# Kernel optimization log

Hardware: AMD Instinct MI355X
Metric: run time of the kernel (lower is better)

The kernel has to match this reference:

```python
import jax, jax.numpy as jnp
import numpy as np
from jax import lax
import math

B, T, CIN, H, W = 8, 64, 2, 64, 64
HID, SPK_C = 32, 64
D_MODEL, N_LAYERS, D_STATE, D_CONV = 512, 4, 16, 4
D_INNER = 2 * D_MODEL
DT_RANK = math.ceil(D_MODEL / 16)  # 32
NUM_CLASSES = 11
FEAT = SPK_C * (H // 4) * (W // 4)  # 16384
BETA, THR = 0.9, 1.0

# --- surrogate-gradient spike (snntorch fast_sigmoid, slope=25) ---
@jax.custom_vjp
def spike_fn(x):
    return (x > 0).astype(x.dtype)

def _spike_fwd(x):
    return spike_fn(x), x

def _spike_bwd(x, g):
    return (g / (25.0 * jnp.abs(x) + 1.0) ** 2,)

spike_fn.defvjp(_spike_fwd, _spike_bwd)

def lif(cur, mem):
    # snntorch Leaky, reset_mechanism='subtract': reset from previous mem (detached)
    reset = lax.stop_gradient((mem > THR).astype(mem.dtype))
    mem = BETA * mem + cur - reset * THR
    spk = spike_fn(mem - THR)
    return spk, mem

def conv2d(x, w, b):
    y = lax.conv_general_dilated(x, w, (1, 1), 'SAME', dimension_numbers=('NCHW', 'OIHW', 'NCHW'))
    return y + b[None, :, None, None]

def maxpool2(x):
    return lax.reduce_window(x, -jnp.inf, lax.max, (1, 1, 2, 2), (1, 1, 2, 2), 'VALID')

def layernorm(x, w, b):
    mu = x.mean(-1, keepdims=True)
    var = ((x - mu) ** 2).mean(-1, keepdims=True)
    return (x - mu) * lax.rsqrt(var + 1e-5) * w + b

def frontend(x, c1w, c1b, c2w, c2b, c3w, c3b):
    mem1 = jnp.zeros((B, HID, H // 2, W // 2), x.dtype)
    mem2 = jnp.zeros((B, HID, H // 4, W // 4), x.dtype)
    mem3 = jnp.zeros((B, SPK_C, H // 4, W // 4), x.dtype)
    def step(carry, xt):
        m1, m2, m3 = carry
        s1, m1 = lif(maxpool2(conv2d(xt, c1w, c1b)), m1)
        s2, m2 = lif(maxpool2(conv2d(s1, c2w, c2b)), m2)
        s3, m3 = lif(conv2d(s2, c3w, c3b), m3)
        return (m1, m2, m3), s3
    _, spk = lax.scan(step, (mem1, mem2, mem3), jnp.swapaxes(x, 0, 1))
    return jnp.swapaxes(spk, 0, 1)  # (B,T,SPK_C,H/4,W/4)

def rate_smooth(a):
    # depthwise conv1d over time with kernel ones(5)/5, padding=2 (moving average)
    Tn = a.shape[1]
    ap = jnp.pad(a, ((0, 0), (2, 2), (0, 0)))
    return sum(ap[:, k:k + Tn, :] for k in range(5)) / 5.0

def mamba_block(x, p):
    ln_w, ln_b, in_w, conv_w, xproj_w, dt_w, dt_b, A_log, Dp, out_w = p
    h = layernorm(x, ln_w, ln_b)
    xr = h @ in_w  # (B,L,2*D_INNER)
    xi, res = jnp.split(xr, 2, axis=-1)
    L = xi.shape[1]
    # causal depthwise conv1d (pad D_CONV-1 left, truncate to L)
    xp = jnp.pad(xi, ((0, 0), (D_CONV - 1, 0), (0, 0)))
    xc = sum(conv_w[:, k] * xp[:, k:k + L, :] for k in range(D_CONV))
    xc = jax.nn.silu(xc)
    x_dbl = xc @ xproj_w  # (B,L,DT_RANK+2*D_STATE)
    dt = x_dbl[..., :DT_RANK]
    Bm = x_dbl[..., DT_RANK:DT_RANK + D_STATE]
    Cm = x_dbl[..., DT_RANK + D_STATE:]
    dt = jax.nn.softplus(dt @ dt_w + dt_b)  # (B,L,D_INNER)
    A = -jnp.exp(A_log)  # (D_INNER,D_STATE)
    dA = jnp.exp(dt[..., None] * A)  # (B,L,D_INNER,D_STATE)
    dBu = dt[..., None] * Bm[:, :, None, :] * xc[..., None]
    def step(hst, inp):
        dA_t, dBu_t, C_t = inp
        hst = dA_t * hst + dBu_t
        return hst, jnp.einsum('bdn,bn->bd', hst, C_t)
    h0 = jnp.zeros((x.shape[0], D_INNER, D_STATE), x.dtype)
    _, ys = lax.scan(step, h0, (jnp.swapaxes(dA, 0, 1), jnp.swapaxes(dBu, 0, 1), jnp.swapaxes(Cm, 0, 1)))
    y = jnp.swapaxes(ys, 0, 1) + xc * Dp
    y = y * jax.nn.silu(res)
    return x + y @ out_w

def _forward(x, c1w, c1b, c2w, c2b, c3w, c3b, inp_w, inp_b, ln_w, ln_b, in_w, conv_w, xproj_w, dt_w, dt_b, A_log, Dp, mb_out_w, fn_w, fn_b, cls_w, cls_b):
    spikes = frontend(x, c1w, c1b, c2w, c2b, c3w, c3b)
    act = rate_smooth(spikes.reshape(B, T, -1))
    h = act @ inp_w + inp_b
    def layer(c, p):
        return mamba_block(c, p), None
    h, _ = lax.scan(layer, h, (ln_w, ln_b, in_w, conv_w, xproj_w, dt_w, dt_b, A_log, Dp, mb_out_w))
    h = h.mean(axis=1)
    h = layernorm(h, fn_w, fn_b)
    return h @ cls_w + cls_b

def setup_inputs():
    key = jax.random.key(0)
    ks = jax.random.split(key, 16)
    def gn(k, shape, scale):
        return jax.random.normal(k, shape, jnp.float32) * scale
    x = jax.random.uniform(ks[0], (B, T, CIN, H, W), jnp.float32)
    c1w = gn(ks[1], (HID, CIN, 3, 3), 1.0 / np.sqrt(CIN * 9)); c1b = jnp.zeros((HID,))
    c2w = gn(ks[2], (HID, HID, 3, 3), 1.0 / np.sqrt(HID * 9)); c2b = jnp.zeros((HID,))
    c3w = gn(ks[3], (SPK_C, HID, 3, 3), 1.0 / np.sqrt(HID * 9)); c3b = jnp.zeros((SPK_C,))
    inp_w = gn(ks[4], (FEAT, D_MODEL), 1.0 / np.sqrt(FEAT)); inp_b = jnp.zeros((D_MODEL,))
    ln_w = jnp.ones((N_LAYERS, D_MODEL)); ln_b = jnp.zeros((N_LAYERS, D_MODEL))
    in_w = gn(ks[5], (N_LAYERS, D_MODEL, 2 * D_INNER), 1.0 / np.sqrt(D_MODEL))
    conv_w = gn(ks[6], (N_LAYERS, D_INNER, D_CONV), 1.0 / np.sqrt(D_CONV))
    xproj_w = gn(ks[7], (N_LAYERS, D_INNER, DT_RANK + 2 * D_STATE), 1.0 / np.sqrt(D_INNER))
    dt_w = gn(ks[8], (N_LAYERS, DT_RANK, D_INNER), 1.0 / np.sqrt(DT_RANK))
    dtv = jnp.exp(jax.random.uniform(ks[9], (N_LAYERS, D_INNER)) * (np.log(0.1) - np.log(0.001)) + np.log(0.001))
    dt_b = dtv + jnp.log(-jnp.expm1(-dtv))
    A_log = jnp.log(jnp.broadcast_to(jnp.arange(1, D_STATE + 1, dtype=jnp.float32), (N_LAYERS, D_INNER, D_STATE))) + jnp.zeros((N_LAYERS, D_INNER, D_STATE))
    Dp = jnp.ones((N_LAYERS, D_INNER))
    mb_out_w = gn(ks[10], (N_LAYERS, D_INNER, D_MODEL), 1.0 / np.sqrt(D_INNER))
    fn_w = jnp.ones((D_MODEL,)); fn_b = jnp.zeros((D_MODEL,))
    cls_w = gn(ks[11], (D_MODEL, NUM_CLASSES), 1.0 / np.sqrt(D_MODEL)); cls_b = jnp.zeros((NUM_CLASSES,))
    return dict(x=x, c1w=c1w, c1b=c1b, c2w=c2w, c2b=c2b, c3w=c3w, c3b=c3b, inp_w=inp_w, inp_b=inp_b, ln_w=ln_w, ln_b=ln_b, in_w=in_w, conv_w=conv_w, xproj_w=xproj_w, dt_w=dt_w, dt_b=dt_b, A_log=A_log, Dp=Dp, mb_out_w=mb_out_w, fn_w=fn_w, fn_b=fn_b, cls_w=cls_w, cls_b=cls_b)

def reference(x, c1w, c1b, c2w, c2b, c3w, c3b, inp_w, inp_b, ln_w, ln_b, in_w, conv_w, xproj_w, dt_w, dt_b, A_log, Dp, mb_out_w, fn_w, fn_b, cls_w, cls_b):
    return _forward(x, c1w, c1b, c2w, c2b, c3w, c3b, inp_w, inp_b, ln_w, ln_b, in_w, conv_w, xproj_w, dt_w, dt_b, A_log, Dp, mb_out_w, fn_w, fn_b, cls_w, cls_b)
```

## Files before the change

### kernel.cpp

```cpp
#include <hip/hip_runtime.h>
#include <math.h>


static constexpr int TT = 64;
static constexpr float BETA = 0.9f, THR = 1.0f;


__global__ __launch_bounds__(256) void k_conv1pool(const float* __restrict__ x,
    const float* __restrict__ w, const float* __restrict__ bias, float* __restrict__ out)
{
    __shared__ float sI[2 * 66 * 76];
    __shared__ float sW[576];
    const int bt = blockIdx.x;
    const int tid = threadIdx.x;
    for (int i = tid; i < 2 * 66 * 76; i += 256) sI[i] = 0.f;
    for (int i = tid; i < 576; i += 256) sW[i] = w[i];
    __syncthreads();
    const float* img = x + (size_t)bt * 8192;
    for (int i = tid; i < 2048; i += 256) {
        float4 v4 = ((const float4*)img)[i];
        int lin = i * 4;
        int ci = lin >> 12, rc = lin & 4095;
        int r = rc >> 6, c = rc & 63;
        *(float4*)&sI[ci * 5016 + (r + 1) * 76 + (c + 4)] = v4;
    }
    __syncthreads();
    const int oh = tid >> 3;
    const int p8 = (tid & 7) * 8;
    float v[2][4][10];
    #pragma unroll
    for (int ci = 0; ci < 2; ++ci) {
        #pragma unroll
        for (int dr = 0; dr < 4; ++dr) {
            const float* rp = &sI[ci * 5016 + (2 * oh + dr) * 76 + p8];
            float2 a  = *(const float2*)&rp[2];
            float4 b4 = *(const float4*)&rp[4];
            float4 c4 = *(const float4*)&rp[8];
            float2 e  = *(const float2*)&rp[12];
            v[ci][dr][0] = a.y;
            v[ci][dr][1] = b4.x; v[ci][dr][2] = b4.y; v[ci][dr][3] = b4.z; v[ci][dr][4] = b4.w;
            v[ci][dr][5] = c4.x; v[ci][dr][6] = c4.y; v[ci][dr][7] = c4.z; v[ci][dr][8] = c4.w;
            v[ci][dr][9] = e.x;
        }
    }
    const int ow0 = (tid & 7) * 4;
    float* obase = out + (size_t)bt * 32768;
    for (int co = 0; co < 32; ++co) {
        float pos[2][8];
        #pragma unroll
        for (int i = 0; i < 2; ++i)
            #pragma unroll
            for (int j = 0; j < 8; ++j) pos[i][j] = 0.f;
        #pragma unroll
        for (int ci = 0; ci < 2; ++ci) {
            const float* wp = &sW[(co * 2 + ci) * 9];
            float w0=wp[0],w1=wp[1],w2=wp[2],w3=wp[3],w4=wp[4],w5=wp[5],w6=wp[6],w7=wp[7],w8=wp[8];
            #pragma unroll
            for (int pr = 0; pr < 2; ++pr)
                #pragma unroll
                for (int pc = 0; pc < 8; ++pc)
                    pos[pr][pc] += v[ci][pr][pc]*w0 + v[ci][pr][pc+1]*w1 + v[ci][pr][pc+2]*w2
                                 + v[ci][pr+1][pc]*w3 + v[ci][pr+1][pc+1]*w4 + v[ci][pr+1][pc+2]*w5
                                 + v[ci][pr+2][pc]*w6 + v[ci][pr+2][pc+1]*w7 + v[ci][pr+2][pc+2]*w8;
        }
        float b0 = bias[co];
        float4 o;
        o.x = fmaxf(fmaxf(pos[0][0], pos[0][1]), fmaxf(pos[1][0], pos[1][1])) + b0;
        o.y = fmaxf(fmaxf(pos[0][2], pos[0][3]), fmaxf(pos[1][2], pos[1][3])) + b0;
        o.z = fmaxf(fmaxf(pos[0][4], pos[0][5]), fmaxf(pos[1][4], pos[1][5])) + b0;
        o.w = fmaxf(fmaxf(pos[0][6], pos[0][7]), fmaxf(pos[1][6], pos[1][7])) + b0;
        *(float4*)&obase[co * 1024 + oh * 32 + ow0] = o;
    }
}

__global__ __launch_bounds__(256) void k_lif(const float* __restrict__ cur,
                                             float* __restrict__ spk, int chw)
{
    int idx = blockIdx.x * 256 + threadIdx.x;
    int b = idx / chw, p = idx % chw;
    const float* cp = cur + (size_t)b * TT * chw + p;
    float* sp = spk + (size_t)b * TT * chw + p;
    float m = 0.f;
    for (int t = 0; t < TT; ++t) {
        float c = cp[(size_t)t * chw];
        float reset = (m > THR) ? THR : 0.f;
        m = BETA * m + c - reset;
        sp[(size_t)t * chw] = (m > THR) ? 1.f : 0.f;
    }
}

__global__ __launch_bounds__(256) void k_conv2(const float* __restrict__ s1,
    const float* __restrict__ w, const float* __restrict__ bias, float* __restrict__ out)
{
    __shared__ float sI[4 * 34 * 40];
    __shared__ float sW2[32 * 8 * 12];
    const int bt = blockIdx.x;
    const int co0 = blockIdx.y * 8;
    const int tid = threadIdx.x;
    for (int i = tid; i < 4 * 34 * 40; i += 256) sI[i] = 0.f;
    for (int i = tid; i < 2304; i += 256) {
        int ci = i / 72, rest = i % 72;
        int co = rest / 9, k = rest % 9;
        sW2[(ci * 8 + co) * 12 + k] = w[((co0 + co) * 32 + ci) * 9 + k];
    }
    const int cc = tid & 31;
    const int g8 = ((tid >> 5) & 3) * 8;
    const int cq = (tid >> 7) * 4;
    float acc[4][8] = {};
    const float* img = s1 + (size_t)bt * 32768;

    float4 pf0, pf1, pf2, pf3;
    auto loadStage = [&](int chunk) {
        const float4* src = (const float4*)(img + chunk * 4096);
        pf0 = src[tid]; pf1 = src[tid + 256]; pf2 = src[tid + 512]; pf3 = src[tid + 768];
    };
    auto writeStage = [&]() {
        #pragma unroll
        for (int j = 0; j < 4; ++j) {
            float4 v4 = (j == 0) ? pf0 : (j == 1) ? pf1 : (j == 2) ? pf2 : pf3;
            int lin = (tid + j * 256) * 4;
            int ci = lin >> 10, rc = lin & 1023;
            int r = rc >> 5, c = rc & 31;
            *(float4*)&sI[ci * 1360 + (r + 1) * 40 + (c + 4)] = v4;
        }
    };

    loadStage(0);
    __syncthreads();
    for (int chunk = 0; chunk < 8; ++chunk) {
        writeStage();
        if (chunk < 7) loadStage(chunk + 1);
        __syncthreads();
        #pragma unroll
        for (int ci4 = 0; ci4 < 4; ++ci4) {
            float win[10][3];
            #pragma unroll
            for (int dr = 0; dr < 10; ++dr) {
                const float* sp = &sI[ci4 * 1360 + (g8 + dr) * 40 + cc + 3];
                win[dr][0] = sp[0]; win[dr][1] = sp[1]; win[dr][2] = sp[2];
            }
            const int ci = chunk * 4 + ci4;
            #pragma unroll
            for (int co = 0; co < 4; ++co) {
                const float4* wq = (const float4*)&sW2[(ci * 8 + cq + co) * 12];
                float4 wa = wq[0], wb = wq[1], wc = wq[2];
                #pragma unroll
                for (int p = 0; p < 8; ++p)
                    acc[co][p] += win[p][0]*wa.x + win[p][1]*wa.y + win[p][2]*wa.z
                                + win[p+1][0]*wa.w + win[p+1][1]*wb.x + win[p+1][2]*wb.y
                                + win[p+2][0]*wb.z + win[p+2][1]*wb.w + win[p+2][2]*wc.x;
            }
        }
        __syncthreads();
    }
    const bool writer = (cc & 1) == 0;
    #pragma unroll
    for (int co = 0; co < 4; ++co) {
        float b0 = bias[co0 + cq + co];
        float* ob = out + (size_t)bt * 8192 + (co0 + cq + co) * 256;
        #pragma unroll
        for (int i = 0; i < 4; ++i) {
            float v = fmaxf(acc[co][2 * i], acc[co][2 * i + 1]);
            v = fmaxf(v, __shfl_xor(v, 1, 64));
            if (writer) ob[(g8 / 2 + i) * 16 + (cc >> 1)] = v + b0;
        }
    }
}

__global__ __launch_bounds__(256) void k_conv3(const float* __restrict__ s2,
    const float* __restrict__ w, const float* __restrict__ bias, float* __restrict__ out)
{
    __shared__ float sI[8 * 18 * 24];
    __shared__ float sW3[8 * 32 * 12];
    const int bt = blockIdx.x;
    const int co0 = blockIdx.y * 32;
    const int tid = threadIdx.x;
    for (int i = tid; i < 8 * 18 * 24; i += 256) sI[i] = 0.f;
    const int cc = tid & 15;
    const int g8 = ((tid >> 4) & 1) * 8;
    const int cq = (tid >> 5) * 4;
    float acc[4][8] = {};
    const float* img = s2 + (size_t)bt * 8192;

    float4 pf0, pf1;
    auto loadStage = [&](int chunk) {
        const float4* src = (const float4*)(img + chunk * 2048);
        pf0 = src[tid]; pf1 = src[tid + 256];
    };
    auto writeStage = [&]() {
        #pragma unroll
        for (int j = 0; j < 2; ++j) {
            float4 v4 = (j == 0) ? pf0 : pf1;
            int lin = (tid + j * 256) * 4;
            int ci = lin >> 8, rc = lin & 255;
            int r = rc >> 4, c = rc & 15;
            *(float4*)&sI[ci * 432 + (r + 1) * 24 + (c + 4)] = v4;
        }
    };

    loadStage(0);
    __syncthreads();
    for (int chunk = 0; chunk < 4; ++chunk) {
        writeStage();
        for (int i = tid; i < 2304; i += 256) {
            int ci = i / 288, rest = i % 288;
            int co = rest / 9, k = rest % 9;
            sW3[(ci * 32 + co) * 12 + k] = w[((co0 + co) * 32 + chunk * 8 + ci) * 9 + k];
        }
        if (chunk < 3) loadStage(chunk + 1);
        __syncthreads();
        #pragma unroll
        for (int ci = 0; ci < 8; ++ci) {
            float win[10][3];
            #pragma unroll
            for (int dr = 0; dr < 10; ++dr) {
                const float* sp = &sI[ci * 432 + (g8 + dr) * 24 + cc + 3];
                win[dr][0] = sp[0]; win[dr][1] = sp[1]; win[dr][2] = sp[2];
            }
            #pragma unroll
            for (int co = 0; co < 4; ++co) {
                const float4* wq = (const float4*)&sW3[(ci * 32 + cq + co) * 12];
                float4 wa = wq[0], wb = wq[1], wc = wq[2];
                #pragma unroll
                for (int p = 0; p < 8; ++p)
                    acc[co][p] += win[p][0]*wa.x + win[p][1]*wa.y + win[p][2]*wa.z
                                + win[p+1][0]*wa.w + win[p+1][1]*wb.x + win[p+1][2]*wb.y
                                + win[p+2][0]*wb.z + win[p+2][1]*wb.w + win[p+2][2]*wc.x;
            }
        }
        __syncthreads();
    }
    #pragma unroll
    for (int co = 0; co < 4; ++co) {
        float b0 = bias[co0 + cq + co];
        float* ob = out + (size_t)bt * 16384 + (co0 + cq + co) * 256;
        #pragma unroll
        for (int p = 0; p < 8; ++p)
            ob[(g8 + p) * 16 + cc] = acc[co][p] + b0;
    }
}

__global__ __launch_bounds__(256) void k_lif3smooth(const float* __restrict__ cur,
                                                    float* __restrict__ act)
{
    int idx = blockIdx.x * 256 + threadIdx.x;
    int b = idx >> 14, f = idx & 16383;
    const float* cp = cur + (size_t)b * TT * 16384 + f;
    float* ap = act + (size_t)b * TT * 16384 + f;
    float m = 0.f;
    float s0 = 0, s1 = 0, s2 = 0, s3 = 0, s4 = 0;
    for (int t = 0; t < TT + 2; ++t) {
        float s = 0.f;
        if (t < TT) {
            float cv = cp[(size_t)t * 16384];
            float reset = (m > THR) ? THR : 0.f;
            m = BETA * m + cv - reset;
            s = (m > THR) ? 1.f : 0.f;
        }
        s4 = s3; s3 = s2; s2 = s1; s1 = s0; s0 = s;
        if (t >= 2) ap[(size_t)(t - 2) * 16384] = (s0 + s1 + s2 + s3 + s4) * 0.2f;
    }
}


__global__ __launch_bounds__(256) void k_gemm(const float* __restrict__ A,
    const float* __restrict__ Bm, float* __restrict__ C, int M, int N, int K)
{
    __shared__ float As[32][68];
    __shared__ float Bs[32][68];
    const int tid = threadIdx.x;
    const int n0 = blockIdx.x * 64, m0 = blockIdx.y * 64;
    const int kchunk = K / gridDim.z;
    const int k0 = blockIdx.z * kchunk, k1 = k0 + kchunk;
    const int ar = tid >> 2, ac = (tid & 3) * 8;
    const int br = tid >> 4, bc = (tid & 15) * 4;
    const int row0 = (tid >> 4) * 4, col0 = (tid & 15) * 4;
    float acc[4][4] = {};
    float4 av0 = *(const float4*)&A[(size_t)(m0 + ar) * K + k0 + ac];
    float4 av1 = *(const float4*)&A[(size_t)(m0 + ar) * K + k0 + ac + 4];
    float4 bv0 = *(const float4*)&Bm[(size_t)(k0 + br) * N + n0 + bc];
    float4 bv1 = *(const float4*)&Bm[(size_t)(k0 + br + 16) * N + n0 + bc];
    for (int kk = k0; kk < k1; kk += 32) {
        As[ac + 0][ar] = av0.x; As[ac + 1][ar] = av0.y;
        As[ac + 2][ar] = av0.z; As[ac + 3][ar] = av0.w;
        As[ac + 4][ar] = av1.x; As[ac + 5][ar] = av1.y;
        As[ac + 6][ar] = av1.z; As[ac + 7][ar] = av1.w;
        *(float4*)&Bs[br][bc] = bv0;
        *(float4*)&Bs[br + 16][bc] = bv1;
        __syncthreads();
        if (kk + 32 < k1) {
            av0 = *(const float4*)&A[(size_t)(m0 + ar) * K + kk + 32 + ac];
            av1 = *(const float4*)&A[(size_t)(m0 + ar) * K + kk + 32 + ac + 4];
            bv0 = *(const float4*)&Bm[(size_t)(kk + 32 + br) * N + n0 + bc];
            bv1 = *(const float4*)&Bm[(size_t)(kk + 32 + br + 16) * N + n0 + bc];
        }
        #pragma unroll
        for (int k = 0; k < 32; ++k) {
            float4 a4 = *(const float4*)&As[k][row0];
            float4 b4 = *(const float4*)&Bs[k][col0];
            acc[0][0] += a4.x * b4.x; acc[0][1] += a4.x * b4.y; acc[0][2] += a4.x * b4.z; acc[0][3] += a4.x * b4.w;
            acc[1][0] += a4.y * b4.x; acc[1][1] += a4.y * b4.y; acc[1][2] += a4.y * b4.z; acc[1][3] += a4.y * b4.w;
            acc[2][0] += a4.z * b4.x; acc[2][1] += a4.z * b4.y; acc[2][2] += a4.z * b4.z; acc[2][3] += a4.z * b4.w;
            acc[3][0] += a4.w * b4.x; acc[3][1] += a4.w * b4.y; acc[3][2] += a4.w * b4.z; acc[3][3] += a4.w * b4.w;
        }
        __syncthreads();
    }
    float* Cp = C + (size_t)blockIdx.z * M * N;
    #pragma unroll
    for (int i = 0; i < 4; ++i) {
        float4 o;
        o.x = acc[i][0]; o.y = acc[i][1]; o.z = acc[i][2]; o.w = acc[i][3];
        *(float4*)&Cp[(size_t)(m0 + row0 + i) * N + n0 + col0] = o;
    }
}

template <bool ADD, bool BIAS>
__global__ __launch_bounds__(256) void k_reduce(const float* __restrict__ part,
    const float* __restrict__ bias, float* __restrict__ out, int MN, int N, int KS)
{
    int i4 = (blockIdx.x * 256 + threadIdx.x) * 4;
    if (i4 >= MN) return;
    float4 v = {0.f, 0.f, 0.f, 0.f};
    for (int z = 0; z < KS; ++z) {
        float4 p = *(const float4*)&part[(size_t)z * MN + i4];
        v.x += p.x; v.y += p.y; v.z += p.z; v.w += p.w;
    }
    if (BIAS) {
        float4 bv = *(const float4*)&bias[i4 % N];
        v.x += bv.x; v.y += bv.y; v.z += bv.z; v.w += bv.w;
    }
    if (ADD) {
        float4 o = *(const float4*)&out[i4];
        v.x += o.x; v.y += o.y; v.z += o.z; v.w += o.w;
    }
    *(float4*)&out[i4] = v;
}


__device__ __forceinline__ float blockSum(float v, float* red)
{
    #pragma unroll
    for (int o = 32; o; o >>= 1) v += __shfl_down(v, o, 64);
    const int wv = threadIdx.x >> 6, lane = threadIdx.x & 63;
    if (lane == 0) red[wv] = v;
    __syncthreads();
    float r = red[0] + red[1] + red[2] + red[3];
    __syncthreads();
    return r;
}

__global__ __launch_bounds__(256) void k_ln(const float* __restrict__ x,
    const float* __restrict__ w, const float* __restrict__ b, float* __restrict__ out)
{
    __shared__ float red[4];
    int row = blockIdx.x;
    const float* xp = x + (size_t)row * 512;
    int c = threadIdx.x * 2;
    float2 v = *(const float2*)&xp[c];
    float mu = blockSum(v.x + v.y, red) * (1.f / 512.f);
    float d0 = v.x - mu, d1 = v.y - mu;
    float var = blockSum(d0 * d0 + d1 * d1, red) * (1.f / 512.f);
    float inv = rsqrtf(var + 1e-5f);
    float2 o;
    o.x = d0 * inv * w[c] + b[c];
    o.y = d1 * inv * w[c + 1] + b[c + 1];
    *(float2*)&out[(size_t)row * 512 + c] = o;
}

__global__ __launch_bounds__(256) void k_convsilu(const float* __restrict__ xr,
    const float* __restrict__ cw, float* __restrict__ xc)
{
    int idx = blockIdx.x * 256 + threadIdx.x;
    int row = idx >> 10;
    int d = idx & 1023;
    int t = row & 63;
    const float* xi = xr + (size_t)(row - t) * 2048 + d;
    float4 w = *(const float4*)&cw[d * 4];
    float a = w.w * xi[(size_t)t * 2048];
    if (t >= 1) a += w.z * xi[(size_t)(t - 1) * 2048];
    if (t >= 2) a += w.y * xi[(size_t)(t - 2) * 2048];
    if (t >= 3) a += w.x * xi[(size_t)(t - 3) * 2048];
    xc[idx] = a / (1.f + __expf(-a));
}

__global__ __launch_bounds__(256) void k_xproj(const float* __restrict__ xc,
    const float* __restrict__ w, float* __restrict__ xdbl)
{
    int row = blockIdx.x * 4 + (threadIdx.x >> 6);
    int col = threadIdx.x & 63;
    const float* a = xc + (size_t)row * 1024;
    float acc = 0.f;
    #pragma unroll 4
    for (int k = 0; k < 1024; k += 4) {
        float4 av = *(const float4*)&a[k];
        acc += av.x * w[(size_t)k * 64 + col] + av.y * w[(size_t)(k + 1) * 64 + col]
             + av.z * w[(size_t)(k + 2) * 64 + col] + av.w * w[(size_t)(k + 3) * 64 + col];
    }
    xdbl[(size_t)row * 64 + col] = acc;
}

__global__ __launch_bounds__(256) void k_dtproj(const float* __restrict__ xdbl,
    const float* __restrict__ w, const float* __restrict__ bias, float* __restrict__ dt)
{
    int idx = blockIdx.x * 256 + threadIdx.x;
    int row = idx >> 10, d = idx & 1023;
    const float* a = xdbl + (size_t)row * 64;
    float acc = bias[d];
    #pragma unroll 8
    for (int r = 0; r < 32; ++r) acc += a[r] * w[(size_t)r * 1024 + d];
    dt[idx] = fmaxf(acc, 0.f) + log1pf(__expf(-fabsf(acc)));
}

__global__ __launch_bounds__(64) void k_scan(const float* __restrict__ dt,
    const float* __restrict__ xc, const float* __restrict__ xdbl,
    const float* __restrict__ xr, const float* __restrict__ A_log,
    const float* __restrict__ Dp, float* __restrict__ y)
{
    const int lane = threadIdx.x & 63;
    const int half = lane >> 5;
    const int p = blockIdx.x * 32 + (lane & 31);
    const int b = p >> 10, d = p & 1023;
    float A[8];
    #pragma unroll
    for (int n = 0; n < 8; ++n) A[n] = -__expf(A_log[d * 16 + half * 8 + n]);
    float Dv = Dp[d];
    float h[8] = {};
    const int row0 = b * 64;
    size_t base = (size_t)row0 * 1024 + d;
    float dtv = dt[base], xv = xc[base];
    float res = xr[(size_t)row0 * 2048 + 1024 + d];
    const float4* Bp = (const float4*)&xdbl[(size_t)row0 * 64 + 32 + half * 8];
    const float4* Cq = (const float4*)&xdbl[(size_t)row0 * 64 + 48 + half * 8];
    float4 B0 = Bp[0], B1 = Bp[1];
    float4 C0 = Cq[0], C1 = Cq[1];
    for (int t = 0; t < TT; ++t) {
        float dtv_n = 0.f, xv_n = 0.f, res_n = 0.f;
        float4 B0n = {}, B1n = {}, C0n = {}, C1n = {};
        if (t < TT - 1) {
            size_t b2 = base + (size_t)(t + 1) * 1024;
            dtv_n = dt[b2]; xv_n = xc[b2];
            res_n = xr[(size_t)(row0 + t + 1) * 2048 + 1024 + d];
            const float4* Bp2 = (const float4*)&xdbl[(size_t)(row0 + t + 1) * 64 + 32 + half * 8];
            const float4* Cq2 = (const float4*)&xdbl[(size_t)(row0 + t + 1) * 64 + 48 + half * 8];
            B0n = Bp2[0]; B1n = Bp2[1]; C0n = Cq2[0]; C1n = Cq2[1];
        }
        float dtx = dtv * xv;
        float acch = 0.f;
        #define SCAN_STEP(Bv, Cv, n0)                                             \
        {                                                                         \
            float bb[4] = {Bv.x, Bv.y, Bv.z, Bv.w};                               \
            float cv[4] = {Cv.x, Cv.y, Cv.z, Cv.w};                               \
            _Pragma("unroll")                                                     \
            for (int r = 0; r < 4; ++r) {                                         \
                int n = n0 + r;                                                   \
                float hv = __expf(dtv * A[n]) * h[n] + dtx * bb[r];               \
                h[n] = hv;                                                        \
                acch += hv * cv[r];                                               \
            }                                                                     \
        }
        SCAN_STEP(B0, C0, 0) SCAN_STEP(B1, C1, 4)
        #undef SCAN_STEP
        float acc = acch + __shfl_xor(acch, 32, 64);
        float sil = res / (1.f + __expf(-res));
        if (half == 0)
            y[(size_t)(row0 + t) * 1024 + d] = (acc + xv * Dv) * sil;
        dtv = dtv_n; xv = xv_n; res = res_n;
        B0 = B0n; B1 = B1n; C0 = C0n; C1 = C1n;
    }
}

__global__ __launch_bounds__(256) void k_meant(const float* __restrict__ h,
                                               float* __restrict__ hm)
{
    int idx = blockIdx.x * 256 + threadIdx.x;
    int b = idx >> 9, d = idx & 511;
    const float* p = h + (size_t)b * 64 * 512 + d;
    float s = 0.f;
    for (int t = 0; t < 64; ++t) s += p[t * 512];
    hm[idx] = s * (1.f / 64.f);
}

__global__ __launch_bounds__(256) void k_final(const float* __restrict__ hm,
    const float* __restrict__ fw, const float* __restrict__ fb,
    const float* __restrict__ cw, const float* __restrict__ cb, float* __restrict__ out)
{
    __shared__ float red[4];
    __shared__ float nrm[512];
    int b = blockIdx.x;
    const float* xp = hm + (size_t)b * 512;
    int c2 = threadIdx.x * 2;
    float2 v = *(const float2*)&xp[c2];
    float mu = blockSum(v.x + v.y, red) * (1.f / 512.f);
    float d0 = v.x - mu, d1 = v.y - mu;
    float var = blockSum(d0 * d0 + d1 * d1, red) * (1.f / 512.f);
    float inv = rsqrtf(var + 1e-5f);
    nrm[c2] = d0 * inv * fw[c2] + fb[c2];
    nrm[c2 + 1] = d1 * inv * fw[c2 + 1] + fb[c2 + 1];
    __syncthreads();
    for (int c = 0; c < 11; ++c) {
        float p = nrm[threadIdx.x] * cw[threadIdx.x * 11 + c]
                + nrm[threadIdx.x + 256] * cw[(threadIdx.x + 256) * 11 + c];
        float s = blockSum(p, red);
        if (threadIdx.x == 0) out[b * 11 + c] = s + cb[c];
    }
}


extern "C" void kernel_launch(void* const* d_in, const int* in_sizes, int n_in,
                              void* d_out, int out_size, void* d_ws, size_t ws_size,
                              hipStream_t stream)
{
    const float* x      = (const float*)d_in[0];
    const float* c1w    = (const float*)d_in[1];
    const float* c1b    = (const float*)d_in[2];
    const float* c2w    = (const float*)d_in[3];
    const float* c2b    = (const float*)d_in[4];
    const float* c3w    = (const float*)d_in[5];
    const float* c3b    = (const float*)d_in[6];
    const float* inp_w  = (const float*)d_in[7];
    const float* inp_b  = (const float*)d_in[8];
    const float* ln_w   = (const float*)d_in[9];
    const float* ln_b   = (const float*)d_in[10];
    const float* in_w   = (const float*)d_in[11];
    const float* conv_w = (const float*)d_in[12];
    const float* xproj_w= (const float*)d_in[13];
    const float* dt_w   = (const float*)d_in[14];
    const float* dt_b   = (const float*)d_in[15];
    const float* A_log  = (const float*)d_in[16];
    const float* Dp     = (const float*)d_in[17];
    const float* mb_out_w=(const float*)d_in[18];
    const float* fn_w   = (const float*)d_in[19];
    const float* fn_b   = (const float*)d_in[20];
    const float* cls_w  = (const float*)d_in[21];
    const float* cls_b  = (const float*)d_in[22];
    float* out = (float*)d_out;

    float* ws   = (float*)d_ws;
    float* bufA = ws;
    float* bufB = bufA + 16777216;
    float* h    = bufB + 16777216;
    float* hn   = h    + 262144;
    float* xr   = hn   + 262144;
    float* xc   = xr   + 1048576;
    float* xdbl = xc   + 524288;
    float* dtb  = xdbl + 32768;
    float* yb   = dtb  + 524288;
    float* hm   = yb   + 524288;

    k_conv1pool<<<512, 256, 0, stream>>>(x, c1w, c1b, bufA);
    k_lif<<<1024, 256, 0, stream>>>(bufA, bufB, 32768);
    k_conv2<<<dim3(512, 4), 256, 0, stream>>>(bufB, c2w, c2b, bufA);
    k_lif<<<256, 256, 0, stream>>>(bufA, bufB, 8192);
    k_conv3<<<dim3(512, 2), 256, 0, stream>>>(bufB, c3w, c3b, bufA);
    k_lif3smooth<<<512, 256, 0, stream>>>(bufA, bufB);

    k_gemm<<<dim3(8, 8, 32), 256, 0, stream>>>(bufB, inp_w, bufA, 512, 512, 16384);
    k_reduce<false, true><<<256, 256, 0, stream>>>(bufA, inp_b, h, 262144, 512, 32);

    for (int l = 0; l < 4; ++l) {
        k_ln<<<512, 256, 0, stream>>>(h, ln_w + l * 512, ln_b + l * 512, hn);
        k_gemm<<<dim3(32, 8, 4), 256, 0, stream>>>(hn, in_w + (size_t)l * 1048576, bufA, 512, 2048, 512);
        k_reduce<false, false><<<1024, 256, 0, stream>>>(bufA, nullptr, xr, 1048576, 2048, 4);
        k_convsilu<<<2048, 256, 0, stream>>>(xr, conv_w + l * 4096, xc);
        k_xproj<<<128, 256, 0, stream>>>(xc, xproj_w + l * 65536, xdbl);
        k_dtproj<<<2048, 256, 0, stream>>>(xdbl, dt_w + l * 32768, dt_b + l * 1024, dtb);
        k_scan<<<256, 64, 0, stream>>>(dtb, xc, xdbl, xr, A_log + l * 16384, Dp + l * 1024, yb);
        k_gemm<<<dim3(8, 8, 16), 256, 0, stream>>>(yb, mb_out_w + (size_t)l * 524288, bufA, 512, 512, 1024);
        k_reduce<true, false><<<256, 256, 0, stream>>>(bufA, nullptr, h, 262144, 512, 16);
    }

    k_meant<<<16, 256, 0, stream>>>(h, hm);
    k_final<<<8, 256, 0, stream>>>(hm, fn_w, fn_b, cls_w, cls_b, out);
}
```

Baseline: 1.032 ms.

## Double-buffer shared-memory input and weight tiles in conv2 and conv3

Converts conv2 and conv3 from single-buffered chunk loops with two barriers per chunk to double-buffered shared memory with one barrier per chunk. Chunks shrink (2 channels in conv2, 4 in conv3), and conv3 also prefetches its weight slices through registers into a second buffer. The aim is to overlap global loads with compute and cut synchronisation, at the cost of more iterations and smaller compute per barrier.

Measured after the change: 1.084 ms. 5.0% more time.

```diff
diff --git a/kernel.cpp b/kernel.cpp
--- a/kernel.cpp
+++ b/kernel.cpp
@@ -92,12 +92,12 @@
 __global__ __launch_bounds__(256) void k_conv2(const float* __restrict__ s1,
     const float* __restrict__ w, const float* __restrict__ bias, float* __restrict__ out)
 {
-    __shared__ float sI[4 * 34 * 40];
+    __shared__ float sI[2][2 * 34 * 40];
     __shared__ float sW2[32 * 8 * 12];
     const int bt = blockIdx.x;
     const int co0 = blockIdx.y * 8;
     const int tid = threadIdx.x;
-    for (int i = tid; i < 4 * 34 * 40; i += 256) sI[i] = 0.f;
+    for (int i = tid; i < 2 * 2720; i += 256) ((float*)sI)[i] = 0.f;
     for (int i = tid; i < 2304; i += 256) {
         int ci = i / 72, rest = i % 72;
         int co = rest / 9, k = rest % 9;
@@ -109,37 +109,38 @@
     float acc[4][8] = {};
     const float* img = s1 + (size_t)bt * 32768;
 
-    float4 pf0, pf1, pf2, pf3;
+    float4 pf0, pf1;
     auto loadStage = [&](int chunk) {
-        const float4* src = (const float4*)(img + chunk * 4096);
-        pf0 = src[tid]; pf1 = src[tid + 256]; pf2 = src[tid + 512]; pf3 = src[tid + 768];
+        const float4* src = (const float4*)(img + chunk * 2048);
+        pf0 = src[tid]; pf1 = src[tid + 256];
     };
-    auto writeStage = [&]() {
-        #pragma unroll
-        for (int j = 0; j < 4; ++j) {
-            float4 v4 = (j == 0) ? pf0 : (j == 1) ? pf1 : (j == 2) ? pf2 : pf3;
+    auto writeStage = [&](int buf) {
+        #pragma unroll
+        for (int j = 0; j < 2; ++j) {
+            float4 v4 = j ? pf1 : pf0;
             int lin = (tid + j * 256) * 4;
             int ci = lin >> 10, rc = lin & 1023;
             int r = rc >> 5, c = rc & 31;
-            *(float4*)&sI[ci * 1360 + (r + 1) * 40 + (c + 4)] = v4;
+            *(float4*)&sI[buf][ci * 1360 + (r + 1) * 40 + (c + 4)] = v4;
         }
     };
 
     loadStage(0);
     __syncthreads();
-    for (int chunk = 0; chunk < 8; ++chunk) {
-        writeStage();
-        if (chunk < 7) loadStage(chunk + 1);
-        __syncthreads();
-        #pragma unroll
-        for (int ci4 = 0; ci4 < 4; ++ci4) {
+    writeStage(0);
+    __syncthreads();
+    loadStage(1);
+    for (int chunk = 0; chunk < 16; ++chunk) {
+        const float* base = sI[chunk & 1];
+        #pragma unroll
+        for (int ci2 = 0; ci2 < 2; ++ci2) {
             float win[10][3];
             #pragma unroll
             for (int dr = 0; dr < 10; ++dr) {
-                const float* sp = &sI[ci4 * 1360 + (g8 + dr) * 40 + cc + 3];
+                const float* sp = &base[ci2 * 1360 + (g8 + dr) * 40 + cc + 3];
                 win[dr][0] = sp[0]; win[dr][1] = sp[1]; win[dr][2] = sp[2];
             }
-            const int ci = chunk * 4 + ci4;
+            const int ci = chunk * 2 + ci2;
             #pragma unroll
             for (int co = 0; co < 4; ++co) {
                 const float4* wq = (const float4*)&sW2[(ci * 8 + cq + co) * 12];
@@ -151,7 +152,11 @@
                                 + win[p+2][0]*wb.z + win[p+2][1]*wb.w + win[p+2][2]*wc.x;
             }
         }
-        __syncthreads();
+        if (chunk < 15) {
+            writeStage((chunk + 1) & 1);
+            __syncthreads();
+            if (chunk + 2 <= 15) loadStage(chunk + 2);
+        }
     }
     const bool writer = (cc & 1) == 0;
     #pragma unroll
@@ -170,56 +175,70 @@
 __global__ __launch_bounds__(256) void k_conv3(const float* __restrict__ s2,
     const float* __restrict__ w, const float* __restrict__ bias, float* __restrict__ out)
 {
-    __shared__ float sI[8 * 18 * 24];
-    __shared__ float sW3[8 * 32 * 12];
+    __shared__ float sI[2][4 * 18 * 24];
+    __shared__ float sW3[2][4 * 32 * 12];
     const int bt = blockIdx.x;
     const int co0 = blockIdx.y * 32;
     const int tid = threadIdx.x;
-    for (int i = tid; i < 8 * 18 * 24; i += 256) sI[i] = 0.f;
+    for (int i = tid; i < 2 * 1728; i += 256) ((float*)sI)[i] = 0.f;
     const int cc = tid & 15;
     const int g8 = ((tid >> 4) & 1) * 8;
     const int cq = (tid >> 5) * 4;
     float acc[4][8] = {};
     const float* img = s2 + (size_t)bt * 8192;
 
-    float4 pf0, pf1;
+    float4 pf0;
+    float pw[5];
     auto loadStage = [&](int chunk) {
-        const float4* src = (const float4*)(img + chunk * 2048);
-        pf0 = src[tid]; pf1 = src[tid + 256];
+        const float4* src = (const float4*)(img + chunk * 1024);
+        pf0 = src[tid];
+        #pragma unroll
+        for (int j = 0; j < 5; ++j) {
+            int i = tid + j * 256;
+            if (i < 1152) {
+                int ci = i / 288, rest = i % 288;
+                int co = rest / 9, k = rest % 9;
+                pw[j] = w[((co0 + co) * 32 + chunk * 4 + ci) * 9 + k];
+            }
+        }
     };
-    auto writeStage = [&]() {
-        #pragma unroll
-        for (int j = 0; j < 2; ++j) {
-            float4 v4 = (j == 0) ? pf0 : pf1;
-            int lin = (tid + j * 256) * 4;
+    auto writeStage = [&](int buf) {
+        {
+            int lin = tid * 4;
             int ci = lin >> 8, rc = lin & 255;
             int r = rc >> 4, c = rc & 15;
-            *(float4*)&sI[ci * 432 + (r + 1) * 24 + (c + 4)] = v4;
+            *(float4*)&sI[buf][ci * 432 + (r + 1) * 24 + (c + 4)] = pf0;
+        }
+        #pragma unroll
+        for (int j = 0; j < 5; ++j) {
+            int i = tid + j * 256;
+            if (i < 1152) {
+                int ci = i / 288, rest = i % 288;
+                int co = rest / 9, k = rest % 9;
+                sW3[buf][(ci * 32 + co) * 12 + k] = pw[j];
+            }
         }
     };
 
     loadStage(0);
     __syncthreads();
-    for (int chunk = 0; chunk < 4; ++chunk) {
-        writeStage();
-        for (int i = tid; i < 2304; i += 256) {
-            int ci = i / 288, rest = i % 288;
-            int co = rest / 9, k = rest % 9;
-            sW3[(ci * 32 + co) * 12 + k] = w[((co0 + co) * 32 + chunk * 8 + ci) * 9 + k];
-        }
-        if (chunk < 3) loadStage(chunk + 1);
-        __syncthreads();
-        #pragma unroll
-        for (int ci = 0; ci < 8; ++ci) {
+    writeStage(0);
+    __syncthreads();
+    loadStage(1);
+    for (int chunk = 0; chunk < 8; ++chunk) {
+        const float* base = sI[chunk & 1];
+        const float* wbase = sW3[chunk & 1];
+        #pragma unroll
+        for (int ci4 = 0; ci4 < 4; ++ci4) {
             float win[10][3];
             #pragma unroll
             for (int dr = 0; dr < 10; ++dr) {
-                const float* sp = &sI[ci * 432 + (g8 + dr) * 24 + cc + 3];
+                const float* sp = &base[ci4 * 432 + (g8 + dr) * 24 + cc + 3];
                 win[dr][0] = sp[0]; win[dr][1] = sp[1]; win[dr][2] = sp[2];
             }
             #pragma unroll
             for (int co = 0; co < 4; ++co) {
-                const float4* wq = (const float4*)&sW3[(ci * 32 + cq + co) * 12];
+                const float4* wq = (const float4*)&wbase[(ci4 * 32 + cq + co) * 12];
                 float4 wa = wq[0], wb = wq[1], wc = wq[2];
                 #pragma unroll
                 for (int p = 0; p < 8; ++p)
@@ -228,7 +247,11 @@
                                 + win[p+2][0]*wb.z + win[p+2][1]*wb.w + win[p+2][2]*wc.x;
             }
         }
-        __syncthreads();
+        if (chunk < 7) {
+            writeStage((chunk + 1) & 1);
+            __syncthreads();
+            if (chunk + 2 <= 7) loadStage(chunk + 2);
+        }
     }
     #pragma unroll
     for (int co = 0; co < 4; ++co) {
```

## Retile conv2 into 2x4 pooled output patches and fuse xproj with dtproj

Applied to the files above, without the earlier changes.

conv2 now gives each thread a 4-row by 2-column output patch instead of an 8-row strip. Each thread then covers a whole 2x2 pool window in registers, which removes the shuffle-based max and the half-idle writer lanes. Fewer input rows are loaded per thread, the shared-memory row pitch is padded to 44, and window reads use float2. Separately, the x-projection and dt-projection kernels are merged into one kernel: each block keeps its 4 xdbl rows in shared memory and computes the full 1024-wide dt with softplus. This saves a launch and an xdbl reload, but dt is now produced by only 128 blocks, each looping 16 times, which lowers parallelism for that stage.

Result: slower. 1.107 ms (+7.2%).

```diff
diff --git a/kernel.cpp b/kernel.cpp
--- a/kernel.cpp
+++ b/kernel.cpp
@@ -92,21 +92,21 @@
 __global__ __launch_bounds__(256) void k_conv2(const float* __restrict__ s1,
     const float* __restrict__ w, const float* __restrict__ bias, float* __restrict__ out)
 {
-    __shared__ float sI[4 * 34 * 40];
+    __shared__ float sI[4 * 34 * 44];
     __shared__ float sW2[32 * 8 * 12];
     const int bt = blockIdx.x;
     const int co0 = blockIdx.y * 8;
     const int tid = threadIdx.x;
-    for (int i = tid; i < 4 * 34 * 40; i += 256) sI[i] = 0.f;
+    for (int i = tid; i < 4 * 34 * 44; i += 256) sI[i] = 0.f;
     for (int i = tid; i < 2304; i += 256) {
         int ci = i / 72, rest = i % 72;
         int co = rest / 9, k = rest % 9;
         sW2[(ci * 8 + co) * 12 + k] = w[((co0 + co) * 32 + ci) * 9 + k];
     }
-    const int cc = tid & 31;
-    const int g8 = ((tid >> 5) & 3) * 8;
+    const int pc = (tid & 15) * 2;
+    const int q4 = ((tid >> 4) & 7) * 4;
     const int cq = (tid >> 7) * 4;
-    float acc[4][8] = {};
+    float acc[4][4][2] = {};
     const float* img = s1 + (size_t)bt * 32768;
 
     float4 pf0, pf1, pf2, pf3;
@@ -121,7 +121,7 @@
             int lin = (tid + j * 256) * 4;
             int ci = lin >> 10, rc = lin & 1023;
             int r = rc >> 5, c = rc & 31;
-            *(float4*)&sI[ci * 1360 + (r + 1) * 40 + (c + 4)] = v4;
+            *(float4*)&sI[ci * 1496 + (r + 1) * 44 + (c + 4)] = v4;
         }
     };
 
@@ -133,11 +133,14 @@
         __syncthreads();
         #pragma unroll
         for (int ci4 = 0; ci4 < 4; ++ci4) {
-            float win[10][3];
+            float win[6][4];
             #pragma unroll
-            for (int dr = 0; dr < 10; ++dr) {
-                const float* sp = &sI[ci4 * 1360 + (g8 + dr) * 40 + cc + 3];
-                win[dr][0] = sp[0]; win[dr][1] = sp[1]; win[dr][2] = sp[2];
+            for (int dr = 0; dr < 6; ++dr) {
+                const float* sp = &sI[ci4 * 1496 + (q4 + dr) * 44 + pc + 2];
+                float2 a = *(const float2*)&sp[0];
+                float2 b = *(const float2*)&sp[2];
+                float2 c = *(const float2*)&sp[4];
+                win[dr][0] = a.y; win[dr][1] = b.x; win[dr][2] = b.y; win[dr][3] = c.x;
             }
             const int ci = chunk * 4 + ci4;
             #pragma unroll
@@ -145,24 +148,27 @@
                 const float4* wq = (const float4*)&sW2[(ci * 8 + cq + co) * 12];
                 float4 wa = wq[0], wb = wq[1], wc = wq[2];
                 #pragma unroll
-                for (int p = 0; p < 8; ++p)
-                    acc[co][p] += win[p][0]*wa.x + win[p][1]*wa.y + win[p][2]*wa.z
-                                + win[p+1][0]*wa.w + win[p+1][1]*wb.x + win[p+1][2]*wb.y
-                                + win[p+2][0]*wb.z + win[p+2][1]*wb.w + win[p+2][2]*wc.x;
+                for (int p = 0; p < 4; ++p) {
+                    acc[co][p][0] += win[p][0]*wa.x + win[p][1]*wa.y + win[p][2]*wa.z
+                                   + win[p+1][0]*wa.w + win[p+1][1]*wb.x + win[p+1][2]*wb.y
+                                   + win[p+2][0]*wb.z + win[p+2][1]*wb.w + win[p+2][2]*wc.x;
+                    acc[co][p][1] += win[p][1]*wa.x + win[p][2]*wa.y + win[p][3]*wa.z
+                                   + win[p+1][1]*wa.w + win[p+1][2]*wb.x + win[p+1][3]*wb.y
+                                   + win[p+2][1]*wb.z + win[p+2][2]*wb.w + win[p+2][3]*wc.x;
+                }
             }
         }
         __syncthreads();
     }
-    const bool writer = (cc & 1) == 0;
     #pragma unroll
     for (int co = 0; co < 4; ++co) {
         float b0 = bias[co0 + cq + co];
         float* ob = out + (size_t)bt * 8192 + (co0 + cq + co) * 256;
         #pragma unroll
-        for (int i = 0; i < 4; ++i) {
-            float v = fmaxf(acc[co][2 * i], acc[co][2 * i + 1]);
-            v = fmaxf(v, __shfl_xor(v, 1, 64));
-            if (writer) ob[(g8 / 2 + i) * 16 + (cc >> 1)] = v + b0;
+        for (int i = 0; i < 2; ++i) {
+            float v = fmaxf(fmaxf(acc[co][2*i][0], acc[co][2*i][1]),
+                            fmaxf(acc[co][2*i+1][0], acc[co][2*i+1][1]));
+            ob[(q4 / 2 + i) * 16 + (pc >> 1)] = v + b0;
         }
     }
 }
@@ -383,32 +389,32 @@
     xc[idx] = a / (1.f + __expf(-a));
 }
 
-__global__ __launch_bounds__(256) void k_xproj(const float* __restrict__ xc,
-    const float* __restrict__ w, float* __restrict__ xdbl)
-{
-    int row = blockIdx.x * 4 + (threadIdx.x >> 6);
-    int col = threadIdx.x & 63;
+__global__ __launch_bounds__(256) void k_xdt(const float* __restrict__ xc,
+    const float* __restrict__ xw, const float* __restrict__ dw,
+    const float* __restrict__ dbias, float* __restrict__ xdbl, float* __restrict__ dt)
+{
+    __shared__ float sx[4][64];
+    const int r = threadIdx.x >> 6;
+    const int row = blockIdx.x * 4 + r;
+    const int col = threadIdx.x & 63;
     const float* a = xc + (size_t)row * 1024;
     float acc = 0.f;
     #pragma unroll 4
     for (int k = 0; k < 1024; k += 4) {
         float4 av = *(const float4*)&a[k];
-        acc += av.x * w[(size_t)k * 64 + col] + av.y * w[(size_t)(k + 1) * 64 + col]
-             + av.z * w[(size_t)(k + 2) * 64 + col] + av.w * w[(size_t)(k + 3) * 64 + col];
-    }
+        acc += av.x * xw[(size_t)k * 64 + col] + av.y * xw[(size_t)(k + 1) * 64 + col]
+             + av.z * xw[(size_t)(k + 2) * 64 + col] + av.w * xw[(size_t)(k + 3) * 64 + col];
+    }
+    sx[r][col] = acc;
     xdbl[(size_t)row * 64 + col] = acc;
-}
-
-__global__ __launch_bounds__(256) void k_dtproj(const float* __restrict__ xdbl,
-    const float* __restrict__ w, const float* __restrict__ bias, float* __restrict__ dt)
-{
-    int idx = blockIdx.x * 256 + threadIdx.x;
-    int row = idx >> 10, d = idx & 1023;
-    const float* a = xdbl + (size_t)row * 64;
-    float acc = bias[d];
-    #pragma unroll 8
-    for (int r = 0; r < 32; ++r) acc += a[r] * w[(size_t)r * 1024 + d];
-    dt[idx] = fmaxf(acc, 0.f) + log1pf(__expf(-fabsf(acc)));
+    __syncthreads();
+    for (int j = 0; j < 16; ++j) {
+        int d = col + j * 64;
+        float s = dbias[d];
+        #pragma unroll 8
+        for (int k = 0; k < 32; ++k) s += sx[r][k] * dw[(size_t)k * 1024 + d];
+        dt[(size_t)row * 1024 + d] = fmaxf(s, 0.f) + log1pf(__expf(-fabsf(s)));
+    }
 }
 
 __global__ __launch_bounds__(64) void k_scan(const float* __restrict__ dt,
@@ -562,8 +568,8 @@
         k_gemm<<<dim3(32, 8, 4), 256, 0, stream>>>(hn, in_w + (size_t)l * 1048576, bufA, 512, 2048, 512);
         k_reduce<false, false><<<1024, 256, 0, stream>>>(bufA, nullptr, xr, 1048576, 2048, 4);
         k_convsilu<<<2048, 256, 0, stream>>>(xr, conv_w + l * 4096, xc);
-        k_xproj<<<128, 256, 0, stream>>>(xc, xproj_w + l * 65536, xdbl);
-        k_dtproj<<<2048, 256, 0, stream>>>(xdbl, dt_w + l * 32768, dt_b + l * 1024, dtb);
+        k_xdt<<<128, 256, 0, stream>>>(xc, xproj_w + l * 65536, dt_w + l * 32768,
+                                       dt_b + l * 1024, xdbl, dtb);
         k_scan<<<256, 64, 0, stream>>>(dtb, xc, xdbl, xr, A_log + l * 16384, Dp + l * 1024, yb);
         k_gemm<<<dim3(8, 8, 16), 256, 0, stream>>>(yb, mb_out_w + (size_t)l * 524288, bufA, 512, 512, 1024);
         k_reduce<true, false><<<256, 256, 0, stream>>>(bufA, nullptr, h, 262144, 512, 16);
```

## Merge output-channel blocks of conv2/conv3 into single larger workgroups

Applied to the files above, without the earlier changes.

Conv2 and conv3 previously split output channels across gridDim.y, so every block reloaded and zero-padded the same input image into shared memory. Now one 1024-thread (conv2) or 512-thread (conv3) workgroup computes all output channels for an image, staging the input once. Weight loads for each chunk are folded into the register prefetch pipeline instead of a separate synchronous loop. This gives fewer blocks and larger workgroups, which may reduce occupancy flexibility and raises register pressure from the per-thread weight index arrays.

After: 1.826 ms. 76.9% more time.

```diff
diff --git a/kernel.cpp b/kernel.cpp
--- a/kernel.cpp
+++ b/kernel.cpp
@@ -89,40 +89,39 @@
     }
 }
 
-__global__ __launch_bounds__(256) void k_conv2(const float* __restrict__ s1,
+__global__ __launch_bounds__(1024) void k_conv2(const float* __restrict__ s1,
     const float* __restrict__ w, const float* __restrict__ bias, float* __restrict__ out)
 {
     __shared__ float sI[4 * 34 * 40];
-    __shared__ float sW2[32 * 8 * 12];
+    __shared__ float sW2[4 * 32 * 12];
     const int bt = blockIdx.x;
-    const int co0 = blockIdx.y * 8;
     const int tid = threadIdx.x;
-    for (int i = tid; i < 4 * 34 * 40; i += 256) sI[i] = 0.f;
-    for (int i = tid; i < 2304; i += 256) {
-        int ci = i / 72, rest = i % 72;
-        int co = rest / 9, k = rest % 9;
-        sW2[(ci * 8 + co) * 12 + k] = w[((co0 + co) * 32 + ci) * 9 + k];
-    }
+    for (int i = tid; i < 4 * 34 * 40; i += 1024) sI[i] = 0.f;
     const int cc = tid & 31;
     const int g8 = ((tid >> 5) & 3) * 8;
     const int cq = (tid >> 7) * 4;
+    const int wi0 = tid;
+    const int w_ci0 = wi0 / 288, w_r0 = wi0 % 288, w_co0 = w_r0 / 9, w_k0 = w_r0 % 9;
+    const int wi1 = tid + 1024;
+    const int w_ci1 = wi1 / 288, w_r1 = wi1 % 288, w_co1 = w_r1 / 9, w_k1 = w_r1 % 9;
+    const bool w1ok = tid < 128;
     float acc[4][8] = {};
     const float* img = s1 + (size_t)bt * 32768;
 
-    float4 pf0, pf1, pf2, pf3;
+    float4 pf;
+    float pw0, pw1;
     auto loadStage = [&](int chunk) {
-        const float4* src = (const float4*)(img + chunk * 4096);
-        pf0 = src[tid]; pf1 = src[tid + 256]; pf2 = src[tid + 512]; pf3 = src[tid + 768];
+        pf = ((const float4*)(img + chunk * 4096))[tid];
+        pw0 = w[(w_co0 * 32 + chunk * 4 + w_ci0) * 9 + w_k0];
+        if (w1ok) pw1 = w[(w_co1 * 32 + chunk * 4 + w_ci1) * 9 + w_k1];
     };
     auto writeStage = [&]() {
-        #pragma unroll
-        for (int j = 0; j < 4; ++j) {
-            float4 v4 = (j == 0) ? pf0 : (j == 1) ? pf1 : (j == 2) ? pf2 : pf3;
-            int lin = (tid + j * 256) * 4;
-            int ci = lin >> 10, rc = lin & 1023;
-            int r = rc >> 5, c = rc & 31;
-            *(float4*)&sI[ci * 1360 + (r + 1) * 40 + (c + 4)] = v4;
-        }
+        int lin = tid * 4;
+        int ci = lin >> 10, rc = lin & 1023;
+        int r = rc >> 5, c = rc & 31;
+        *(float4*)&sI[ci * 1360 + (r + 1) * 40 + (c + 4)] = pf;
+        sW2[(w_ci0 * 32 + w_co0) * 12 + w_k0] = pw0;
+        if (w1ok) sW2[(w_ci1 * 32 + w_co1) * 12 + w_k1] = pw1;
     };
 
     loadStage(0);
@@ -139,10 +138,9 @@
                 const float* sp = &sI[ci4 * 1360 + (g8 + dr) * 40 + cc + 3];
                 win[dr][0] = sp[0]; win[dr][1] = sp[1]; win[dr][2] = sp[2];
             }
-            const int ci = chunk * 4 + ci4;
             #pragma unroll
             for (int co = 0; co < 4; ++co) {
-                const float4* wq = (const float4*)&sW2[(ci * 8 + cq + co) * 12];
+                const float4* wq = (const float4*)&sW2[(ci4 * 32 + cq + co) * 12];
                 float4 wa = wq[0], wb = wq[1], wc = wq[2];
                 #pragma unroll
                 for (int p = 0; p < 8; ++p)
@@ -156,8 +154,8 @@
     const bool writer = (cc & 1) == 0;
     #pragma unroll
     for (int co = 0; co < 4; ++co) {
-        float b0 = bias[co0 + cq + co];
-        float* ob = out + (size_t)bt * 8192 + (co0 + cq + co) * 256;
+        float b0 = bias[cq + co];
+        float* ob = out + (size_t)bt * 8192 + (cq + co) * 256;
         #pragma unroll
         for (int i = 0; i < 4; ++i) {
             float v = fmaxf(acc[co][2 * i], acc[co][2 * i + 1]);
@@ -167,46 +165,50 @@
     }
 }
 
-__global__ __launch_bounds__(256) void k_conv3(const float* __restrict__ s2,
+__global__ __launch_bounds__(512) void k_conv3(const float* __restrict__ s2,
     const float* __restrict__ w, const float* __restrict__ bias, float* __restrict__ out)
 {
     __shared__ float sI[8 * 18 * 24];
-    __shared__ float sW3[8 * 32 * 12];
+    __shared__ float sW3[8 * 64 * 12];
     const int bt = blockIdx.x;
-    const int co0 = blockIdx.y * 32;
     const int tid = threadIdx.x;
-    for (int i = tid; i < 8 * 18 * 24; i += 256) sI[i] = 0.f;
+    for (int i = tid; i < 8 * 18 * 24; i += 512) sI[i] = 0.f;
     const int cc = tid & 15;
     const int g8 = ((tid >> 4) & 1) * 8;
     const int cq = (tid >> 5) * 4;
+    int w_ci[9], w_co[9], w_k[9];
+    #pragma unroll
+    for (int j = 0; j < 9; ++j) {
+        int i = tid + j * 512;
+        w_ci[j] = i / 576;
+        int rest = i % 576;
+        w_co[j] = rest / 9; w_k[j] = rest % 9;
+    }
     float acc[4][8] = {};
     const float* img = s2 + (size_t)bt * 8192;
 
-    float4 pf0, pf1;
+    float4 pf;
+    float pw[9];
     auto loadStage = [&](int chunk) {
-        const float4* src = (const float4*)(img + chunk * 2048);
-        pf0 = src[tid]; pf1 = src[tid + 256];
+        pf = ((const float4*)(img + chunk * 2048))[tid];
+        #pragma unroll
+        for (int j = 0; j < 9; ++j)
+            pw[j] = w[(w_co[j] * 32 + chunk * 8 + w_ci[j]) * 9 + w_k[j]];
     };
     auto writeStage = [&]() {
-        #pragma unroll
-        for (int j = 0; j < 2; ++j) {
-            float4 v4 = (j == 0) ? pf0 : pf1;
-            int lin = (tid + j * 256) * 4;
-            int ci = lin >> 8, rc = lin & 255;
-            int r = rc >> 4, c = rc & 15;
-            *(float4*)&sI[ci * 432 + (r + 1) * 24 + (c + 4)] = v4;
-        }
+        int lin = tid * 4;
+        int ci = lin >> 8, rc = lin & 255;
+        int r = rc >> 4, c = rc & 15;
+        *(float4*)&sI[ci * 432 + (r + 1) * 24 + (c + 4)] = pf;
+        #pragma unroll
+        for (int j = 0; j < 9; ++j)
+            sW3[(w_ci[j] * 64 + w_co[j]) * 12 + w_k[j]] = pw[j];
     };
 
     loadStage(0);
     __syncthreads();
     for (int chunk = 0; chunk < 4; ++chunk) {
         writeStage();
-        for (int i = tid; i < 2304; i += 256) {
-            int ci = i / 288, rest = i % 288;
-            int co = rest / 9, k = rest % 9;
-            sW3[(ci * 32 + co) * 12 + k] = w[((co0 + co) * 32 + chunk * 8 + ci) * 9 + k];
-        }
         if (chunk < 3) loadStage(chunk + 1);
         __syncthreads();
         #pragma unroll
@@ -219,7 +221,7 @@
             }
             #pragma unroll
             for (int co = 0; co < 4; ++co) {
-                const float4* wq = (const float4*)&sW3[(ci * 32 + cq + co) * 12];
+                const float4* wq = (const float4*)&sW3[(ci * 64 + cq + co) * 12];
                 float4 wa = wq[0], wb = wq[1], wc = wq[2];
                 #pragma unroll
                 for (int p = 0; p < 8; ++p)
@@ -232,8 +234,8 @@
     }
     #pragma unroll
     for (int co = 0; co < 4; ++co) {
-        float b0 = bias[co0 + cq + co];
-        float* ob = out + (size_t)bt * 16384 + (co0 + cq + co) * 256;
+        float b0 = bias[cq + co];
+        float* ob = out + (size_t)bt * 16384 + (cq + co) * 256;
         #pragma unroll
         for (int p = 0; p < 8; ++p)
             ob[(g8 + p) * 16 + cc] = acc[co][p] + b0;
@@ -549,9 +551,9 @@
 
     k_conv1pool<<<512, 256, 0, stream>>>(x, c1w, c1b, bufA);
     k_lif<<<1024, 256, 0, stream>>>(bufA, bufB, 32768);
-    k_conv2<<<dim3(512, 4), 256, 0, stream>>>(bufB, c2w, c2b, bufA);
+    k_conv2<<<512, 1024, 0, stream>>>(bufB, c2w, c2b, bufA);
     k_lif<<<256, 256, 0, stream>>>(bufA, bufB, 8192);
-    k_conv3<<<dim3(512, 2), 256, 0, stream>>>(bufB, c3w, c3b, bufA);
+    k_conv3<<<512, 512, 0, stream>>>(bufB, c3w, c3b, bufA);
     k_lif3smooth<<<512, 256, 0, stream>>>(bufA, bufB);
 
     k_gemm<<<dim3(8, 8, 32), 256, 0, stream>>>(bufB, inp_w, bufA, 512, 512, 16384);
```
